# Kernel optimization log

Measured on AMD Instinct MI355X. Metric: run time of the kernel, lower is better.

Reference implementation:

```python
import jax, jax.numpy as jnp
import numpy as np

DT = 0.001  # fixed dt in SimplifiedSSM.forward
LN_EPS = 1e-5


def _layernorm(x, g, b):
    m = jnp.mean(x, axis=-1, keepdims=True)
    v = jnp.mean(jnp.square(x - m), axis=-1, keepdims=True)
    return (x - m) * jax.lax.rsqrt(v + LN_EPS) * g + b


def setup_inputs() -> dict:
    key = jax.random.key(0)
    ks = jax.random.split(key, 12)
    Bn, C, H, W = 8, 1024, 32, 32
    depth, S = 4, 128
    d = C
    inp = {
        "x": jax.random.normal(ks[0], (Bn, C, H, W), dtype=jnp.float32),
        # SSM params, stacked over depth. A scaled by 0.1 for numerical stability
        # of the length-1024 recurrence (same math, tamer eigenvalues).
        "A": 0.1 * jax.random.normal(ks[1], (depth, S, S), dtype=jnp.float32),
        "Bp": jax.random.normal(ks[2], (depth, S, d), dtype=jnp.float32),
        "Cp": jax.random.normal(ks[3], (depth, d, S), dtype=jnp.float32),
        "Dp": jax.random.normal(ks[4], (depth, d), dtype=jnp.float32),
        # Linear layers (PyTorch convention: y = x @ W.T + b)
        "Wi": jax.random.normal(ks[5], (depth, d, d), dtype=jnp.float32) / np.sqrt(d),
        "bi": jax.random.normal(ks[6], (depth, d), dtype=jnp.float32) * 0.01,
        "Wo": jax.random.normal(ks[7], (depth, d, d), dtype=jnp.float32) / np.sqrt(d),
        "bo": jax.random.normal(ks[8], (depth, d), dtype=jnp.float32) * 0.01,
        # LayerNorm affine params
        "gamma": jnp.ones((depth, d), dtype=jnp.float32),
        "beta": jnp.zeros((depth, d), dtype=jnp.float32),
    }
    return inp


def reference(x, A, Bp, Cp, Dp, Wi, bi, Wo, bo, gamma, beta):
    Bn, C, H, W = x.shape
    depth, S, _ = A.shape
    # b c h w -> b (h w) c
    seq = x.reshape(Bn, C, H * W).transpose(0, 2, 1)
    eye = jnp.eye(S, dtype=x.dtype)
    for i in range(depth):
        n = _layernorm(seq, gamma[i], beta[i])
        u = n @ Wi[i].T + bi[i]                       # (B, L, d)
        A_bar = eye + DT * A[i]                       # (S, S)
        ub = jnp.einsum('bld,sd->lbs', u, DT * Bp[i]) # (L, B, S)

        def step(h, ub_t):
            h = h @ A_bar.T + ub_t
            return h, h

        h0 = jnp.zeros((Bn, S), dtype=x.dtype)
        _, hs = jax.lax.scan(step, h0, ub)            # hs: (L, B, S)
        y = jnp.einsum('lbs,ds->bld', hs, Cp[i]) + u * Dp[i]
        seq = seq + y @ Wo[i].T + bo[i]
    return seq.transpose(0, 2, 1).reshape(Bn, C, H, W)
```

## Files before the change

kernel.cpp:

```cpp
#include <hip/hip_runtime.h>
#include <stdint.h>

#define DT_STEP 0.001f
#define LN_EPS  1e-5f
#define Bn      8
#define Lseq    1024
#define Dm      1024
#define Sn      128
#define DEPTH   4
#define Mrows   (Bn * Lseq)
#define Qc      32
#define NCHUNK  (Lseq / Qc)
#define NPOW    33

typedef short bf16x8 __attribute__((ext_vector_type(8)));
typedef float f32x4  __attribute__((ext_vector_type(4)));

__device__ __forceinline__ unsigned short f2bf(float f) {
    unsigned int u = __float_as_uint(f);
    u += 0x7fffu + ((u >> 16) & 1u);
    return (unsigned short)(u >> 16);
}

#define GLOAD_LDS16(gp, lp)                                                \
    __builtin_amdgcn_global_load_lds(                                      \
        (const __attribute__((address_space(1))) unsigned int*)(gp),       \
        (__attribute__((address_space(3))) unsigned int*)(lp), 16, 0, 0)

__global__ __launch_bounds__(256) void f2bf_kernel(const float* __restrict__ src,
                                                   unsigned short* __restrict__ dst,
                                                   int n) {
    int i = (blockIdx.x * 256 + threadIdx.x) * 4;
    if (i < n) {
        float4 v = *(const float4*)(src + i);
        ushort4 o;
        o.x = f2bf(v.x); o.y = f2bf(v.y); o.z = f2bf(v.z); o.w = f2bf(v.w);
        *(ushort4*)(dst + i) = o;
    }
}

__global__ __launch_bounds__(256) void convscale_kernel(const float* __restrict__ Wo,
                                                        const float* __restrict__ Dp,
                                                        unsigned short* __restrict__ dst) {
    int z = blockIdx.y;
    int i = (blockIdx.x * 256 + threadIdx.x) * 4;
    const float* S = Wo + (size_t)z * Dm * Dm;
    const float* dp = Dp + (size_t)z * Dm;
    float4 v = *(const float4*)(S + i);
    int c = i & (Dm - 1);
    float4 d = *(const float4*)(dp + c);
    ushort4 o;
    o.x = f2bf(v.x * d.x); o.y = f2bf(v.y * d.y);
    o.z = f2bf(v.z * d.z); o.w = f2bf(v.w * d.w);
    *(ushort4*)(dst + (size_t)z * Dm * Dm + i) = o;
}

__global__ __launch_bounds__(256) void transpose_f2bf(const float* __restrict__ src,
                                                      unsigned short* __restrict__ dst,
                                                      int R, int C) {
    __shared__ float t[32][33];
    int z = blockIdx.z;
    const float* S = src + (size_t)z * R * C;
    unsigned short* D = dst + (size_t)z * R * C;
    int r0 = blockIdx.y * 32, c0 = blockIdx.x * 32;
    int tx = threadIdx.x & 31, ty = threadIdx.x >> 5;
    for (int rr = ty; rr < 32; rr += 8)
        t[rr][tx] = S[(size_t)(r0 + rr) * C + c0 + tx];
    __syncthreads();
    for (int rr = ty; rr < 32; rr += 8)
        D[(size_t)(c0 + rr) * R + r0 + tx] = f2bf(t[tx][rr]);
}

__global__ __launch_bounds__(256) void c2dt_kernel(const float* __restrict__ Bp,
                                                   const float* __restrict__ bi,
                                                   float* __restrict__ c2dt) {
    int z = blockIdx.x, s = blockIdx.y;
    int tid = threadIdx.x;
    const float* br = Bp + ((size_t)z * Sn + s) * Dm;
    const float* bb = bi + (size_t)z * Dm;
    float4 v = *(const float4*)(br + tid * 4);
    float4 w = *(const float4*)(bb + tid * 4);
    float acc = v.x * w.x + v.y * w.y + v.z * w.z + v.w * w.w;
#pragma unroll
    for (int off = 32; off > 0; off >>= 1) acc += __shfl_down(acc, off, 64);
    __shared__ float red[4];
    if ((tid & 63) == 0) red[tid >> 6] = acc;
    __syncthreads();
    if (tid == 0) c2dt[z * Sn + s] = DT_STEP * (red[0] + red[1] + red[2] + red[3]);
}

__global__ __launch_bounds__(256) void boeff_kernel(const float* __restrict__ Wo,
                                                    const float* __restrict__ Dp,
                                                    const float* __restrict__ bi,
                                                    const float* __restrict__ bo,
                                                    float* __restrict__ boeff) {
    int z = blockIdx.x, c = blockIdx.y;
    int tid = threadIdx.x;
    const float* wr = Wo + ((size_t)z * Dm + c) * Dm;
    const float* dp = Dp + (size_t)z * Dm;
    const float* bb = bi + (size_t)z * Dm;
    float4 w = *(const float4*)(wr + tid * 4);
    float4 d = *(const float4*)(dp + tid * 4);
    float4 b = *(const float4*)(bb + tid * 4);
    float acc = w.x * d.x * b.x + w.y * d.y * b.y + w.z * d.z * b.z + w.w * d.w * b.w;
#pragma unroll
    for (int off = 32; off > 0; off >>= 1) acc += __shfl_down(acc, off, 64);
    __shared__ float red[4];
    if ((tid & 63) == 0) red[tid >> 6] = acc;
    __syncthreads();
    if (tid == 0)
        boeff[(size_t)z * Dm + c] =
            bo[(size_t)z * Dm + c] + red[0] + red[1] + red[2] + red[3];
}

__global__ __launch_bounds__(1024) void transpose_bll(const float* __restrict__ src,
                                                      float* __restrict__ dst) {
    __shared__ float tile[32][33];
    int b  = blockIdx.z;
    int i0 = blockIdx.y * 32, j0 = blockIdx.x * 32;
    int tx = threadIdx.x, ty = threadIdx.y;
    const float* S = src + (size_t)b * Dm * Lseq;
    float*       D = dst + (size_t)b * Dm * Lseq;
    tile[ty][tx] = S[(size_t)(j0 + ty) * 1024 + i0 + tx];
    __syncthreads();
    D[(size_t)(i0 + ty) * 1024 + j0 + tx] = tile[tx][ty];
}

__global__ __launch_bounds__(256) void ln_kernel(const float* __restrict__ x,
                                                 unsigned short* __restrict__ outp,
                                                 const float* __restrict__ g,
                                                 const float* __restrict__ bta) {
    int row = blockIdx.x;
    int tid = threadIdx.x;
    const float* xr = x + (size_t)row * Dm;
    float4 v = *(const float4*)(xr + tid * 4);
    float s  = v.x + v.y + v.z + v.w;
    float ss = v.x * v.x + v.y * v.y + v.z * v.z + v.w * v.w;
#pragma unroll
    for (int off = 32; off > 0; off >>= 1) {
        s  += __shfl_down(s, off, 64);
        ss += __shfl_down(ss, off, 64);
    }
    __shared__ float red[8];
    __shared__ float mv[2];
    int wave = tid >> 6, lane = tid & 63;
    if (lane == 0) { red[wave] = s; red[4 + wave] = ss; }
    __syncthreads();
    if (tid == 0) {
        float st  = red[0] + red[1] + red[2] + red[3];
        float sst = red[4] + red[5] + red[6] + red[7];
        float mean = st / (float)Dm;
        float var  = sst / (float)Dm - mean * mean;
        mv[0] = mean;
        mv[1] = rsqrtf(var + LN_EPS);
    }
    __syncthreads();
    float mean = mv[0], rstd = mv[1];
    int c = tid * 4;
    float4 gv = *(const float4*)(g + c);
    float4 bv = *(const float4*)(bta + c);
    ushort4 o;
    o.x = f2bf((v.x - mean) * rstd * gv.x + bv.x);
    o.y = f2bf((v.y - mean) * rstd * gv.y + bv.y);
    o.z = f2bf((v.z - mean) * rstd * gv.z + bv.z);
    o.w = f2bf((v.w - mean) * rstd * gv.w + bv.w);
    *(ushort4*)(outp + (size_t)row * Dm + c) = o;
}

__global__ __launch_bounds__(512) void gemm_bk64(
    const unsigned short* __restrict__ A1, int sA1,
    const unsigned short* __restrict__ A2, int sA2, int KA1,
    const unsigned short* __restrict__ B1, int sB1,
    const unsigned short* __restrict__ B2, int sB2,
    float* __restrict__ Cf, unsigned short* __restrict__ Ch,
    const float* __restrict__ bias1, const float* __restrict__ bias2,
    int ny, int N, int K, float scale, int mode,
    long batchA, long batchB, long batchC) {
    __shared__ __align__(16) unsigned short As[1024 * 8];
    __shared__ __align__(16) unsigned short Bs[1024 * 8];
    int flat = blockIdx.x;
    int rb = flat % ny, cb = flat / ny;
    int row0 = rb * 128, col0 = cb * 128;
    int z = blockIdx.y;
    int tid  = threadIdx.x;
    int wave = tid >> 6, lane = tid & 63;
    int wm = (wave & 1) * 64, wn = (wave >> 1) * 32;
    int lr = lane & 15, lq = lane >> 4;

    int rowS[2], kclS[2], slotOff[2];
#pragma unroll
    for (int q = 0; q < 2; q++) {
        int s = tid + q * 512;
        rowS[q] = s >> 3;
        kclS[q] = (s & 7) ^ ((s >> 3) & 7);
        slotOff[q] = s * 8;
    }
    int aoff[4][2], boff[2][2];
#pragma unroll
    for (int i = 0; i < 4; i++)
#pragma unroll
        for (int h = 0; h < 2; h++) {
            int ra = wm + i * 16 + lr;
            aoff[i][h] = (ra * 8 + ((lq + 4 * h) ^ (ra & 7))) * 8;
        }
#pragma unroll
    for (int j = 0; j < 2; j++)
#pragma unroll
        for (int h = 0; h < 2; h++) {
            int rn = wn + j * 16 + lr;
            boff[j][h] = (rn * 8 + ((lq + 4 * h) ^ (rn & 7))) * 8;
        }

    const unsigned short* A1b = A1 + (size_t)z * batchA;
    const unsigned short* BfixBlk = nullptr;
    int sBfix = sB1;
    if (mode == 0) {
        if (col0 < N - 128) { BfixBlk = B1 + (size_t)col0 * sB1; sBfix = sB1; }
        else                { BfixBlk = B2;                      sBfix = sB2; }
    } else if (mode == 2) {
        BfixBlk = B1 + (size_t)z * batchB + (size_t)col0 * sB1;
        sBfix = sB1;
    }

    f32x4 acc[4][2];
#pragma unroll
    for (int i = 0; i < 4; i++)
#pragma unroll
        for (int j = 0; j < 2; j++) acc[i][j] = (f32x4){0.f, 0.f, 0.f, 0.f};

    for (int k0 = 0; k0 < K; k0 += 64) {
        const unsigned short *Ab, *Bb;
        int sa, sb, ko;
        if (mode == 1) {
            if (k0 < KA1) { Ab = A1; sa = sA1; Bb = B1 + (size_t)col0 * sB1; sb = sB1; ko = k0; }
            else          { Ab = A2; sa = sA2; Bb = B2 + (size_t)col0 * sB2; sb = sB2; ko = k0 - KA1; }
        } else {
            Ab = A1b; sa = sA1; Bb = BfixBlk; sb = sBfix; ko = k0;
        }
        const unsigned short* Abr = Ab + (size_t)row0 * sa + ko;
        const unsigned short* Bbr = Bb + ko;
        __syncthreads();
#pragma unroll
        for (int q = 0; q < 2; q++) {
            GLOAD_LDS16(Abr + (size_t)rowS[q] * sa + kclS[q] * 8, &As[slotOff[q]]);
            GLOAD_LDS16(Bbr + (size_t)rowS[q] * sb + kclS[q] * 8, &Bs[slotOff[q]]);
        }
        __syncthreads();
#pragma unroll
        for (int h = 0; h < 2; h++) {
            bf16x8 af[4], bfr[2];
#pragma unroll
            for (int i = 0; i < 4; i++) af[i]  = *(const bf16x8*)&As[aoff[i][h]];
#pragma unroll
            for (int j = 0; j < 2; j++) bfr[j] = *(const bf16x8*)&Bs[boff[j][h]];
#pragma unroll
            for (int i = 0; i < 4; i++)
#pragma unroll
                for (int j = 0; j < 2; j++)
                    acc[i][j] = __builtin_amdgcn_mfma_f32_16x16x32_bf16(af[i], bfr[j],
                                                                       acc[i][j], 0, 0, 0);
        }
    }
#pragma unroll
    for (int i = 0; i < 4; i++) {
#pragma unroll
        for (int j = 0; j < 2; j++) {
#pragma unroll
            for (int r = 0; r < 4; r++) {
                int row = row0 + wm + i * 16 + lq * 4 + r;
                int col = col0 + wn + j * 16 + lr;
                float v = acc[i][j][r];
                if (mode == 0) {
                    int nu = N - 128;
                    if (col < nu) {
                        Ch[(size_t)row * nu + col] = f2bf(v + bias1[col]);
                    } else {
                        int cc = col - nu;
                        Cf[(size_t)row * 128 + cc] = v + bias2[cc];
                    }
                } else if (mode == 1) {
                    size_t idx = (size_t)row * N + col;
                    Cf[idx] = Cf[idx] + v + bias1[col];
                } else {
                    Ch[(size_t)z * batchC + (size_t)row * N + col] = f2bf(v * scale);
                }
            }
        }
    }
}

__global__ __launch_bounds__(128) void pow_init(const float* __restrict__ Amat,
                                                float* __restrict__ Pow) {
    int i = blockIdx.x;
    int s = blockIdx.y;
    int k = threadIdx.x;
    float eye = (s == k) ? 1.f : 0.f;
    size_t base = (size_t)i * NPOW * (Sn * Sn);
    Pow[base + (size_t)s * Sn + k] = eye;
    Pow[base + (size_t)(Sn * Sn) + (size_t)s * Sn + k] =
        eye + DT_STEP * Amat[(size_t)i * Sn * Sn + (size_t)s * Sn + k];
}

__global__ __launch_bounds__(256) void pow_mul(float* __restrict__ Pow, int m, int kmax) {
    int job = blockIdx.z;
    int i  = job / kmax;
    int kk = job % kmax + 1;
    const float* Pa = Pow + ((size_t)i * NPOW + m) * (Sn * Sn);
    const float* Pb = Pow + ((size_t)i * NPOW + kk) * (Sn * Sn);
    float*       Pc = Pow + ((size_t)i * NPOW + m + kk) * (Sn * Sn);
    int r0 = blockIdx.y * 64, c0 = blockIdx.x * 32;
    __shared__ float Asl[64 * 129];
    __shared__ float Bsl[128 * 32];
    int tx = threadIdx.x, ty = threadIdx.y;
    int tid = ty * 16 + tx;
    for (int idx = tid; idx < 64 * 128; idx += 256) {
        int r = idx >> 7, cc = idx & 127;
        Asl[r * 129 + cc] = Pa[(size_t)(r0 + r) * 128 + cc];
    }
    for (int idx = tid; idx < 128 * 32; idx += 256) {
        int r = idx >> 5, cc = idx & 31;
        Bsl[r * 32 + cc] = Pb[(size_t)r * 128 + c0 + cc];
    }
    __syncthreads();
    float acc[4][2] = {{0.f,0.f},{0.f,0.f},{0.f,0.f},{0.f,0.f}};
    for (int k = 0; k < 128; k++) {
        float b0 = Bsl[k * 32 + tx * 2];
        float b1 = Bsl[k * 32 + tx * 2 + 1];
#pragma unroll
        for (int r = 0; r < 4; r++) {
            float a = Asl[(ty * 4 + r) * 129 + k];
            acc[r][0] += a * b0;
            acc[r][1] += a * b1;
        }
    }
#pragma unroll
    for (int r = 0; r < 4; r++) {
        Pc[(size_t)(r0 + ty * 4 + r) * 128 + c0 + tx * 2]     = acc[r][0];
        Pc[(size_t)(r0 + ty * 4 + r) * 128 + c0 + tx * 2 + 1] = acc[r][1];
    }
}

__global__ __launch_bounds__(128) void local_scan(const float* __restrict__ ub,
                                                  float* __restrict__ hs,
                                                  const float* __restrict__ Abar) {
    int b = blockIdx.x / NCHUNK;
    int c = blockIdx.x % NCHUNK;
    int s = threadIdx.x;
    float arow[Sn];
#pragma unroll
    for (int k = 0; k < Sn; k += 4) {
        float4 v = *(const float4*)(Abar + (size_t)s * Sn + k);
        arow[k] = v.x; arow[k + 1] = v.y; arow[k + 2] = v.z; arow[k + 3] = v.w;
    }
    __shared__ __align__(16) float hsh[Sn];
    hsh[s] = 0.f;
    __syncthreads();
    size_t base = (size_t)(b * Lseq + c * Qc) * Sn + s;
    for (int t = 0; t < Qc; t++) {
        float ut = ub[base + (size_t)t * Sn];
        float a0 = 0.f, a1 = 0.f, a2 = 0.f, a3 = 0.f;
#pragma unroll
        for (int k = 0; k < Sn; k += 16) {
            float4 h0 = *(const float4*)&hsh[k];
            float4 h1 = *(const float4*)&hsh[k + 4];
            float4 h2 = *(const float4*)&hsh[k + 8];
            float4 h3 = *(const float4*)&hsh[k + 12];
            a0 += arow[k + 0] * h0.x + arow[k + 1] * h0.y + arow[k + 2] * h0.z + arow[k + 3] * h0.w;
            a1 += arow[k + 4] * h1.x + arow[k + 5] * h1.y + arow[k + 6] * h1.z + arow[k + 7] * h1.w;
            a2 += arow[k + 8] * h2.x + arow[k + 9] * h2.y + arow[k + 10] * h2.z + arow[k + 11] * h2.w;
            a3 += arow[k + 12] * h3.x + arow[k + 13] * h3.y + arow[k + 14] * h3.z + arow[k + 15] * h3.w;
        }
        float hv = ut + (a0 + a1) + (a2 + a3);
        hs[base + (size_t)t * Sn] = hv;
        __syncthreads();
        hsh[s] = hv;
        __syncthreads();
    }
}

__global__ __launch_bounds__(128) void carry_scan(const float* __restrict__ hs,
                                                  const float* __restrict__ AQ,
                                                  float* __restrict__ carry) {
    int b = blockIdx.x;
    int s = threadIdx.x;
    float le[NCHUNK];
#pragma unroll
    for (int c = 0; c < NCHUNK; c++)
        le[c] = hs[(size_t)(b * Lseq + c * Qc + Qc - 1) * Sn + s];
    float arow[Sn];
#pragma unroll
    for (int k = 0; k < Sn; k += 4) {
        float4 v = *(const float4*)(AQ + (size_t)s * Sn + k);
        arow[k] = v.x; arow[k + 1] = v.y; arow[k + 2] = v.z; arow[k + 3] = v.w;
    }
    __shared__ __align__(16) float csh[Sn];
    csh[s] = 0.f;
    __syncthreads();
    for (int c = 0; c < NCHUNK; c++) {
        carry[((size_t)b * NCHUNK + c) * Sn + s] = csh[s];
        float a0 = 0.f, a1 = 0.f, a2 = 0.f, a3 = 0.f;
#pragma unroll
        for (int k = 0; k < Sn; k += 16) {
            float4 h0 = *(const float4*)&csh[k];
            float4 h1 = *(const float4*)&csh[k + 4];
            float4 h2 = *(const float4*)&csh[k + 8];
            float4 h3 = *(const float4*)&csh[k + 12];
            a0 += arow[k + 0] * h0.x + arow[k + 1] * h0.y + arow[k + 2] * h0.z + arow[k + 3] * h0.w;
            a1 += arow[k + 4] * h1.x + arow[k + 5] * h1.y + arow[k + 6] * h1.z + arow[k + 7] * h1.w;
            a2 += arow[k + 8] * h2.x + arow[k + 9] * h2.y + arow[k + 10] * h2.z + arow[k + 11] * h2.w;
            a3 += arow[k + 12] * h3.x + arow[k + 13] * h3.y + arow[k + 14] * h3.z + arow[k + 15] * h3.w;
        }
        float cv = le[c] + (a0 + a1) + (a2 + a3);
        __syncthreads();
        csh[s] = cv;
        __syncthreads();
    }
}

__global__ __launch_bounds__(256) void fixup_scan(const float* __restrict__ hs,
                                                  unsigned short* __restrict__ hs_bf,
                                                  const float* __restrict__ PowLayer,
                                                  const float* __restrict__ carry) {
    int t  = blockIdx.x;
    int c4 = blockIdx.y;
    const float* P = PowLayer + (size_t)(t + 1) * (Sn * Sn);
    __shared__ float Pl[Sn * 65];
    __shared__ float cl[4][Bn * Sn];
    int tid = threadIdx.x;
#pragma unroll
    for (int cc = 0; cc < 4; cc++)
        for (int idx = tid; idx < Bn * Sn; idx += 256)
            cl[cc][idx] = carry[((size_t)(idx >> 7) * NCHUNK + (c4 * 4 + cc)) * Sn + (idx & 127)];
    int s = tid & 127, bh = tid >> 7;
    float acc[4][4];
#pragma unroll
    for (int cc = 0; cc < 4; cc++)
#pragma unroll
        for (int j = 0; j < 4; j++) acc[cc][j] = 0.f;
    for (int kh = 0; kh < 2; kh++) {
        __syncthreads();
        for (int idx = tid; idx < Sn * 64; idx += 256) {
            int r = idx >> 6, kk = idx & 63;
            Pl[r * 65 + kk] = P[(size_t)r * Sn + kh * 64 + kk];
        }
        __syncthreads();
        for (int kk = 0; kk < 64; kk++) {
            float pw = Pl[s * 65 + kk];
            int kg = kh * 64 + kk;
#pragma unroll
            for (int cc = 0; cc < 4; cc++)
#pragma unroll
                for (int j = 0; j < 4; j++)
                    acc[cc][j] += pw * cl[cc][(bh * 4 + j) * Sn + kg];
        }
    }
#pragma unroll
    for (int cc = 0; cc < 4; cc++) {
        int c = c4 * 4 + cc;
#pragma unroll
        for (int j = 0; j < 4; j++) {
            int bb = bh * 4 + j;
            size_t rowi = (size_t)(bb * Lseq + c * Qc + t) * Sn + s;
            hs_bf[rowi] = f2bf(hs[rowi] + acc[cc][j]);
        }
    }
}

extern "C" void kernel_launch(void* const* d_in, const int* in_sizes, int n_in,
                              void* d_out, int out_size, void* d_ws, size_t ws_size,
                              hipStream_t stream) {
    const float* x     = (const float*)d_in[0];
    const float* Am    = (const float*)d_in[1];
    const float* Bp    = (const float*)d_in[2];
    const float* Cp    = (const float*)d_in[3];
    const float* Dp    = (const float*)d_in[4];
    const float* Wi    = (const float*)d_in[5];
    const float* bi    = (const float*)d_in[6];
    const float* Wo    = (const float*)d_in[7];
    const float* bo    = (const float*)d_in[8];
    const float* gamma = (const float*)d_in[9];
    const float* beta  = (const float*)d_in[10];
    float* out = (float*)d_out;
    (void)in_sizes; (void)n_in; (void)out_size; (void)ws_size;

    char* ws = (char*)d_ws;
    float*          seq   = (float*)(ws + (size_t)0);
    unsigned short* nbuf  = (unsigned short*)(ws + (size_t)33554432);
    unsigned short* WiTh  = (unsigned short*)(ws + (size_t)33554432);
    unsigned short* Woh   = (unsigned short*)(ws + (size_t)41943040);
    unsigned short* W4h   = (unsigned short*)(ws + (size_t)50331648);
    float*          boeff = (float*)(ws + (size_t)58720256);
    float*          ub    = (float*)(ws + (size_t)67108864);
    float*          hs    = (float*)(ws + (size_t)71303168);
    unsigned short* hs_bf = (unsigned short*)(ws + (size_t)75497472);
    float*          Pow   = (float*)(ws + (size_t)77594624);
    float*          carry = (float*)(ws + (size_t)86245376);
    unsigned short* Wo2h  = (unsigned short*)(ws + (size_t)94765056);
    unsigned short* Bph   = (unsigned short*)(ws + (size_t)103153664);
    unsigned short* CpTh  = (unsigned short*)(ws + (size_t)104202240);
    unsigned short* M2h   = (unsigned short*)(ws + (size_t)105250816);
    unsigned short* W3h   = (unsigned short*)(ws + (size_t)106299392);
    float*          c2dt  = (float*)(ws + (size_t)107347968);

    const long WW = (long)Dm * Dm;
    const long SW = (long)Sn * Dm;

    hipLaunchKernelGGL(f2bf_kernel, dim3(DEPTH * WW / 1024), dim3(256), 0, stream,
                       Wo, Woh, DEPTH * (int)WW);
    hipLaunchKernelGGL(f2bf_kernel, dim3(DEPTH * SW / 1024), dim3(256), 0, stream,
                       Bp, Bph, DEPTH * (int)SW);
    hipLaunchKernelGGL(convscale_kernel, dim3(WW / 1024, DEPTH), dim3(256), 0, stream,
                       Wo, Dp, Wo2h);
    hipLaunchKernelGGL(transpose_f2bf, dim3(32, 32, DEPTH), dim3(256), 0, stream,
                       Wi, WiTh, Dm, Dm);
    hipLaunchKernelGGL(transpose_f2bf, dim3(4, 32, DEPTH), dim3(256), 0, stream,
                       Cp, CpTh, Dm, Sn);
    hipLaunchKernelGGL(c2dt_kernel, dim3(DEPTH, Sn), dim3(256), 0, stream, Bp, bi, c2dt);
    hipLaunchKernelGGL(boeff_kernel, dim3(DEPTH, Dm), dim3(256), 0, stream,
                       Wo, Dp, bi, bo, boeff);

    hipLaunchKernelGGL(gemm_bk64, dim3(8, DEPTH), dim3(512), 0, stream,
                       Bph, Dm, (const unsigned short*)nullptr, 0, 0,
                       WiTh, Dm, (const unsigned short*)nullptr, 0,
                       (float*)nullptr, M2h, (const float*)nullptr, (const float*)nullptr,
                       1, Dm, Dm, DT_STEP, 2, SW, WW, SW);
    hipLaunchKernelGGL(gemm_bk64, dim3(8, DEPTH), dim3(512), 0, stream,
                       Woh, Dm, (const unsigned short*)nullptr, 0, 0,
                       CpTh, Dm, (const unsigned short*)nullptr, 0,
                       (float*)nullptr, W3h, (const float*)nullptr, (const float*)nullptr,
                       8, Sn, Dm, 1.f, 2, WW, SW, SW);
    hipLaunchKernelGGL(gemm_bk64, dim3(8 * 8, DEPTH), dim3(512), 0, stream,
                       Wo2h, Dm, (const unsigned short*)nullptr, 0, 0,
                       WiTh, Dm, (const unsigned short*)nullptr, 0,
                       (float*)nullptr, W4h, (const float*)nullptr, (const float*)nullptr,
                       8, Dm, Dm, 1.f, 2, WW, WW, WW);

    hipLaunchKernelGGL(transpose_bll, dim3(32, 32, Bn), dim3(32, 32), 0, stream, x, seq);

    hipLaunchKernelGGL(pow_init, dim3(DEPTH, Sn), dim3(Sn), 0, stream, Am, Pow);
    for (int m = 1; m < Qc; m <<= 1) {
        hipLaunchKernelGGL(pow_mul, dim3(4, 2, DEPTH * m), dim3(16, 16), 0, stream,
                           Pow, m, m);
    }

    for (int i = 0; i < DEPTH; i++) {
        const unsigned short* M2_i = M2h + (size_t)i * SW;
        const unsigned short* W3_i = W3h + (size_t)i * SW;
        const unsigned short* W4_i = W4h + (size_t)i * WW;
        const float* PowL = Pow + (size_t)i * NPOW * (Sn * Sn);

        hipLaunchKernelGGL(ln_kernel, dim3(Mrows), dim3(256), 0, stream,
                           seq, nbuf, gamma + i * Dm, beta + i * Dm);
        hipLaunchKernelGGL(gemm_bk64, dim3(64, 1), dim3(512), 0, stream,
                           nbuf, Dm, (const unsigned short*)nullptr, 0, 0,
                           (const unsigned short*)nullptr, 0, M2_i, Dm,
                           ub, (unsigned short*)nullptr, bi + i * Dm, c2dt + i * Sn,
                           64, Sn, Dm, 1.f, 0, 0, 0, 0);
        hipLaunchKernelGGL(local_scan, dim3(Bn * NCHUNK), dim3(Sn), 0, stream,
                           ub, hs, PowL + (size_t)1 * Sn * Sn);
        hipLaunchKernelGGL(carry_scan, dim3(Bn), dim3(Sn), 0, stream,
                           hs, PowL + (size_t)Qc * Sn * Sn, carry);
        hipLaunchKernelGGL(fixup_scan, dim3(Qc, NCHUNK / 4), dim3(256), 0, stream,
                           hs, hs_bf, PowL, carry);
        hipLaunchKernelGGL(gemm_bk64, dim3(8 * 64, 1), dim3(512), 0, stream,
                           hs_bf, Sn, nbuf, Dm, Sn,
                           W3_i, Sn, W4_i, Dm,
                           seq, (unsigned short*)nullptr, boeff + i * Dm, (const float*)nullptr,
                           64, Dm, Dm + Sn, 1.f, 1, 0, 0, 0);
    }

    hipLaunchKernelGGL(transpose_bll, dim3(32, 32, Bn), dim3(32, 32), 0, stream, seq, out);
}
```

Before: 810.7 us.

## Fuse LayerNorm, ub projection GEMM and local chunk scan into one kernel

Replaces the per-layer ln_kernel, the ub GEMM and local_scan with one fused kernel. Each 128-row block computes LN statistics, normalizes into LDS while writing nbuf, runs the 128x128 MFMA projection, and performs the four 32-step chunk scans straight from LDS. This drops the ub round trip through global memory and two launches per layer. The setup conversion and bias kernels are also merged to cut launch count. The fused kernel runs only 64 blocks with large LDS use, so the GPU may be underfilled compared with the separate launches.

After: 891.7 us. 1.1x slower.

```diff
diff --git a/kernel.cpp b/kernel.cpp
--- a/kernel.cpp
+++ b/kernel.cpp
@@ -27,32 +27,33 @@
         (const __attribute__((address_space(1))) unsigned int*)(gp),       \
         (__attribute__((address_space(3))) unsigned int*)(lp), 16, 0, 0)
 
-__global__ __launch_bounds__(256) void f2bf_kernel(const float* __restrict__ src,
-                                                   unsigned short* __restrict__ dst,
-                                                   int n) {
-    int i = (blockIdx.x * 256 + threadIdx.x) * 4;
-    if (i < n) {
-        float4 v = *(const float4*)(src + i);
+__global__ __launch_bounds__(256) void prep_conv(const float* __restrict__ Wo,
+                                                 const float* __restrict__ Dp,
+                                                 const float* __restrict__ Bp,
+                                                 unsigned short* __restrict__ Woh,
+                                                 unsigned short* __restrict__ Wo2h,
+                                                 unsigned short* __restrict__ Bph) {
+    int z = blockIdx.y;
+    int bx = blockIdx.x;
+    if (bx < 1024) {
+        int i = (bx * 256 + threadIdx.x) * 4;
+        const float* S = Wo + (size_t)z * Dm * Dm;
+        float4 v = *(const float4*)(S + i);
+        int c = i & (Dm - 1);
+        float4 d = *(const float4*)(Dp + (size_t)z * Dm + c);
+        ushort4 o1, o2;
+        o1.x = f2bf(v.x); o1.y = f2bf(v.y); o1.z = f2bf(v.z); o1.w = f2bf(v.w);
+        o2.x = f2bf(v.x * d.x); o2.y = f2bf(v.y * d.y);
+        o2.z = f2bf(v.z * d.z); o2.w = f2bf(v.w * d.w);
+        *(ushort4*)(Woh  + (size_t)z * Dm * Dm + i) = o1;
+        *(ushort4*)(Wo2h + (size_t)z * Dm * Dm + i) = o2;
+    } else {
+        int i = ((bx - 1024) * 256 + threadIdx.x) * 4;
+        float4 v = *(const float4*)(Bp + (size_t)z * Sn * Dm + i);
         ushort4 o;
         o.x = f2bf(v.x); o.y = f2bf(v.y); o.z = f2bf(v.z); o.w = f2bf(v.w);
-        *(ushort4*)(dst + i) = o;
-    }
-}
-
-__global__ __launch_bounds__(256) void convscale_kernel(const float* __restrict__ Wo,
-                                                        const float* __restrict__ Dp,
-                                                        unsigned short* __restrict__ dst) {
-    int z = blockIdx.y;
-    int i = (blockIdx.x * 256 + threadIdx.x) * 4;
-    const float* S = Wo + (size_t)z * Dm * Dm;
-    const float* dp = Dp + (size_t)z * Dm;
-    float4 v = *(const float4*)(S + i);
-    int c = i & (Dm - 1);
-    float4 d = *(const float4*)(dp + c);
-    ushort4 o;
-    o.x = f2bf(v.x * d.x); o.y = f2bf(v.y * d.y);
-    o.z = f2bf(v.z * d.z); o.w = f2bf(v.w * d.w);
-    *(ushort4*)(dst + (size_t)z * Dm * Dm + i) = o;
+        *(ushort4*)(Bph + (size_t)z * Sn * Dm + i) = o;
+    }
 }
 
 __global__ __launch_bounds__(256) void transpose_f2bf(const float* __restrict__ src,
@@ -71,46 +72,42 @@
         D[(size_t)(c0 + rr) * R + r0 + tx] = f2bf(t[tx][rr]);
 }
 
-__global__ __launch_bounds__(256) void c2dt_kernel(const float* __restrict__ Bp,
-                                                   const float* __restrict__ bi,
-                                                   float* __restrict__ c2dt) {
-    int z = blockIdx.x, s = blockIdx.y;
+__global__ __launch_bounds__(256) void c2dt_boeff(const float* __restrict__ Bp,
+                                                  const float* __restrict__ bi,
+                                                  const float* __restrict__ Wo,
+                                                  const float* __restrict__ Dp,
+                                                  const float* __restrict__ bo,
+                                                  float* __restrict__ c2dt,
+                                                  float* __restrict__ boeff) {
+    int z = blockIdx.x, j = blockIdx.y;
     int tid = threadIdx.x;
-    const float* br = Bp + ((size_t)z * Sn + s) * Dm;
-    const float* bb = bi + (size_t)z * Dm;
-    float4 v = *(const float4*)(br + tid * 4);
-    float4 w = *(const float4*)(bb + tid * 4);
-    float acc = v.x * w.x + v.y * w.y + v.z * w.z + v.w * w.w;
+    float acc;
+    if (j < Sn) {
+        const float* br = Bp + ((size_t)z * Sn + j) * Dm;
+        const float* bb = bi + (size_t)z * Dm;
+        float4 v = *(const float4*)(br + tid * 4);
+        float4 w = *(const float4*)(bb + tid * 4);
+        acc = v.x * w.x + v.y * w.y + v.z * w.z + v.w * w.w;
+    } else {
+        int c = j - Sn;
+        const float* wr = Wo + ((size_t)z * Dm + c) * Dm;
+        const float* dp = Dp + (size_t)z * Dm;
+        const float* bb = bi + (size_t)z * Dm;
+        float4 w = *(const float4*)(wr + tid * 4);
+        float4 d = *(const float4*)(dp + tid * 4);
+        float4 b = *(const float4*)(bb + tid * 4);
+        acc = w.x * d.x * b.x + w.y * d.y * b.y + w.z * d.z * b.z + w.w * d.w * b.w;
+    }
 #pragma unroll
     for (int off = 32; off > 0; off >>= 1) acc += __shfl_down(acc, off, 64);
     __shared__ float red[4];
     if ((tid & 63) == 0) red[tid >> 6] = acc;
     __syncthreads();
-    if (tid == 0) c2dt[z * Sn + s] = DT_STEP * (red[0] + red[1] + red[2] + red[3]);
-}
-
-__global__ __launch_bounds__(256) void boeff_kernel(const float* __restrict__ Wo,
-                                                    const float* __restrict__ Dp,
-                                                    const float* __restrict__ bi,
-                                                    const float* __restrict__ bo,
-                                                    float* __restrict__ boeff) {
-    int z = blockIdx.x, c = blockIdx.y;
-    int tid = threadIdx.x;
-    const float* wr = Wo + ((size_t)z * Dm + c) * Dm;
-    const float* dp = Dp + (size_t)z * Dm;
-    const float* bb = bi + (size_t)z * Dm;
-    float4 w = *(const float4*)(wr + tid * 4);
-    float4 d = *(const float4*)(dp + tid * 4);
-    float4 b = *(const float4*)(bb + tid * 4);
-    float acc = w.x * d.x * b.x + w.y * d.y * b.y + w.z * d.z * b.z + w.w * d.w * b.w;
-#pragma unroll
-    for (int off = 32; off > 0; off >>= 1) acc += __shfl_down(acc, off, 64);
-    __shared__ float red[4];
-    if ((tid & 63) == 0) red[tid >> 6] = acc;
-    __syncthreads();
-    if (tid == 0)
-        boeff[(size_t)z * Dm + c] =
-            bo[(size_t)z * Dm + c] + red[0] + red[1] + red[2] + red[3];
+    if (tid == 0) {
+        float tot = red[0] + red[1] + red[2] + red[3];
+        if (j < Sn) c2dt[z * Sn + j] = DT_STEP * tot;
+        else        boeff[(size_t)z * Dm + (j - Sn)] = bo[(size_t)z * Dm + (j - Sn)] + tot;
+    }
 }
 
 __global__ __launch_bounds__(1024) void transpose_bll(const float* __restrict__ src,
@@ -126,45 +123,175 @@
     D[(size_t)(i0 + ty) * 1024 + j0 + tx] = tile[tx][ty];
 }
 
-__global__ __launch_bounds__(256) void ln_kernel(const float* __restrict__ x,
-                                                 unsigned short* __restrict__ outp,
-                                                 const float* __restrict__ g,
-                                                 const float* __restrict__ bta) {
-    int row = blockIdx.x;
-    int tid = threadIdx.x;
-    const float* xr = x + (size_t)row * Dm;
-    float4 v = *(const float4*)(xr + tid * 4);
-    float s  = v.x + v.y + v.z + v.w;
-    float ss = v.x * v.x + v.y * v.y + v.z * v.z + v.w * v.w;
-#pragma unroll
-    for (int off = 32; off > 0; off >>= 1) {
-        s  += __shfl_down(s, off, 64);
-        ss += __shfl_down(ss, off, 64);
-    }
-    __shared__ float red[8];
-    __shared__ float mv[2];
+__global__ __launch_bounds__(512) void fused_front(
+    const float* __restrict__ seq,
+    unsigned short* __restrict__ nbuf,
+    float* __restrict__ hs,
+    const unsigned short* __restrict__ M2,
+    const float* __restrict__ gam,
+    const float* __restrict__ bet,
+    const float* __restrict__ c2dtL,
+    const float* __restrict__ Abar) {
+    __shared__ __align__(16) unsigned short As[1024 * 8];
+    __shared__ __align__(16) unsigned short Bs[1024 * 8];
+    __shared__ __align__(16) float ubl[128 * 129];
+    __shared__ float mrow[128], rrow[128], cdt[128];
+    __shared__ __align__(16) float hsh[4 * 128];
+
+    int beta = blockIdx.x;
+    int row0 = beta * 128;
+    int tid  = threadIdx.x;
     int wave = tid >> 6, lane = tid & 63;
-    if (lane == 0) { red[wave] = s; red[4 + wave] = ss; }
+    int wm = (wave & 1) * 64, wn = (wave >> 1) * 32;
+    int lr = lane & 15, lq = lane >> 4;
+
+    {
+        int r = tid >> 2, q = tid & 3;
+        const float* xr = seq + (size_t)(row0 + r) * Dm;
+        float s = 0.f, ss = 0.f;
+        for (int j = 0; j < 64; j++) {
+            float4 v = *(const float4*)(xr + j * 16 + q * 4);
+            s  += v.x + v.y + v.z + v.w;
+            ss += v.x * v.x + v.y * v.y + v.z * v.z + v.w * v.w;
+        }
+        s  += __shfl_xor(s, 1, 64);  ss += __shfl_xor(ss, 1, 64);
+        s  += __shfl_xor(s, 2, 64);  ss += __shfl_xor(ss, 2, 64);
+        if (q == 0) {
+            float mean = s / (float)Dm;
+            float var  = ss / (float)Dm - mean * mean;
+            mrow[r] = mean;
+            rrow[r] = rsqrtf(var + LN_EPS);
+        }
+        if (tid < 128) cdt[tid] = c2dtL[tid];
+    }
+
+    int rowS[2], kclS[2], slotOff[2];
+#pragma unroll
+    for (int q = 0; q < 2; q++) {
+        int s = tid + q * 512;
+        rowS[q] = s >> 3;
+        kclS[q] = (s & 7) ^ ((s >> 3) & 7);
+        slotOff[q] = s * 8;
+    }
+    int aoff[4][2], boff[2][2];
+#pragma unroll
+    for (int i = 0; i < 4; i++)
+#pragma unroll
+        for (int h = 0; h < 2; h++) {
+            int ra = wm + i * 16 + lr;
+            aoff[i][h] = (ra * 8 + ((lq + 4 * h) ^ (ra & 7))) * 8;
+        }
+#pragma unroll
+    for (int j = 0; j < 2; j++)
+#pragma unroll
+        for (int h = 0; h < 2; h++) {
+            int rn = wn + j * 16 + lr;
+            boff[j][h] = (rn * 8 + ((lq + 4 * h) ^ (rn & 7))) * 8;
+        }
+
+    f32x4 acc[4][2];
+#pragma unroll
+    for (int i = 0; i < 4; i++)
+#pragma unroll
+        for (int j = 0; j < 2; j++) acc[i][j] = (f32x4){0.f, 0.f, 0.f, 0.f};
+
+    for (int k0 = 0; k0 < Dm; k0 += 64) {
+        __syncthreads();
+#pragma unroll
+        for (int q = 0; q < 2; q++)
+            GLOAD_LDS16(M2 + (size_t)rowS[q] * Dm + k0 + kclS[q] * 8, &Bs[slotOff[q]]);
+#pragma unroll
+        for (int q = 0; q < 2; q++) {
+            int gi = tid * 2 + q;
+            int rA = gi >> 3, kc = gi & 7;
+            int col = k0 + kc * 8;
+            const float* p = seq + (size_t)(row0 + rA) * Dm + col;
+            float4 v0 = *(const float4*)(p);
+            float4 v1 = *(const float4*)(p + 4);
+            float m = mrow[rA], rs = rrow[rA];
+            float4 g0 = *(const float4*)(gam + col);
+            float4 g1 = *(const float4*)(gam + col + 4);
+            float4 b0 = *(const float4*)(bet + col);
+            float4 b1 = *(const float4*)(bet + col + 4);
+            bf16x8 pk;
+            pk[0] = (short)f2bf((v0.x - m) * rs * g0.x + b0.x);
+            pk[1] = (short)f2bf((v0.y - m) * rs * g0.y + b0.y);
+            pk[2] = (short)f2bf((v0.z - m) * rs * g0.z + b0.z);
+            pk[3] = (short)f2bf((v0.w - m) * rs * g0.w + b0.w);
+            pk[4] = (short)f2bf((v1.x - m) * rs * g1.x + b1.x);
+            pk[5] = (short)f2bf((v1.y - m) * rs * g1.y + b1.y);
+            pk[6] = (short)f2bf((v1.z - m) * rs * g1.z + b1.z);
+            pk[7] = (short)f2bf((v1.w - m) * rs * g1.w + b1.w);
+            int slot = rA * 8 + (kc ^ (rA & 7));
+            *(bf16x8*)&As[slot * 8] = pk;
+            *(bf16x8*)(nbuf + (size_t)(row0 + rA) * Dm + col) = pk;
+        }
+        __syncthreads();
+#pragma unroll
+        for (int h = 0; h < 2; h++) {
+            bf16x8 af[4], bfr[2];
+#pragma unroll
+            for (int i = 0; i < 4; i++) af[i]  = *(const bf16x8*)&As[aoff[i][h]];
+#pragma unroll
+            for (int j = 0; j < 2; j++) bfr[j] = *(const bf16x8*)&Bs[boff[j][h]];
+#pragma unroll
+            for (int i = 0; i < 4; i++)
+#pragma unroll
+                for (int j = 0; j < 2; j++)
+                    acc[i][j] = __builtin_amdgcn_mfma_f32_16x16x32_bf16(af[i], bfr[j],
+                                                                       acc[i][j], 0, 0, 0);
+        }
+    }
+
+#pragma unroll
+    for (int i = 0; i < 4; i++)
+#pragma unroll
+        for (int j = 0; j < 2; j++)
+#pragma unroll
+            for (int r = 0; r < 4; r++) {
+                int rl = wm + i * 16 + lq * 4 + r;
+                int cl = wn + j * 16 + lr;
+                ubl[rl * 129 + cl] = acc[i][j][r] + cdt[cl];
+            }
+    {
+        int s = tid & 127, cc = tid >> 7;
+        hsh[cc * 128 + s] = 0.f;
+    }
     __syncthreads();
-    if (tid == 0) {
-        float st  = red[0] + red[1] + red[2] + red[3];
-        float sst = red[4] + red[5] + red[6] + red[7];
-        float mean = st / (float)Dm;
-        float var  = sst / (float)Dm - mean * mean;
-        mv[0] = mean;
-        mv[1] = rsqrtf(var + LN_EPS);
-    }
-    __syncthreads();
-    float mean = mv[0], rstd = mv[1];
-    int c = tid * 4;
-    float4 gv = *(const float4*)(g + c);
-    float4 bv = *(const float4*)(bta + c);
-    ushort4 o;
-    o.x = f2bf((v.x - mean) * rstd * gv.x + bv.x);
-    o.y = f2bf((v.y - mean) * rstd * gv.y + bv.y);
-    o.z = f2bf((v.z - mean) * rstd * gv.z + bv.z);
-    o.w = f2bf((v.w - mean) * rstd * gv.w + bv.w);
-    *(ushort4*)(outp + (size_t)row * Dm + c) = o;
+
+    {
+        int s = tid & 127, cc = tid >> 7;
+        float arow[Sn];
+#pragma unroll
+        for (int k = 0; k < Sn; k += 4) {
+            float4 v = *(const float4*)(Abar + (size_t)s * Sn + k);
+            arow[k] = v.x; arow[k + 1] = v.y; arow[k + 2] = v.z; arow[k + 3] = v.w;
+        }
+        int b = beta >> 3;
+        int c = (beta & 7) * 4 + cc;
+        size_t gbase = (size_t)(b * Lseq + c * Qc) * Sn + s;
+        float* hch = &hsh[cc * 128];
+        for (int t = 0; t < Qc; t++) {
+            float ut = ubl[(cc * 32 + t) * 129 + s];
+            float a0 = 0.f, a1 = 0.f, a2 = 0.f, a3 = 0.f;
+#pragma unroll
+            for (int k = 0; k < Sn; k += 16) {
+                float4 h0 = *(const float4*)&hch[k];
+                float4 h1 = *(const float4*)&hch[k + 4];
+                float4 h2 = *(const float4*)&hch[k + 8];
+                float4 h3 = *(const float4*)&hch[k + 12];
+                a0 += arow[k + 0] * h0.x + arow[k + 1] * h0.y + arow[k + 2] * h0.z + arow[k + 3] * h0.w;
+                a1 += arow[k + 4] * h1.x + arow[k + 5] * h1.y + arow[k + 6] * h1.z + arow[k + 7] * h1.w;
+                a2 += arow[k + 8] * h2.x + arow[k + 9] * h2.y + arow[k + 10] * h2.z + arow[k + 11] * h2.w;
+                a3 += arow[k + 12] * h3.x + arow[k + 13] * h3.y + arow[k + 14] * h3.z + arow[k + 15] * h3.w;
+            }
+            float hv = ut + (a0 + a1) + (a2 + a3);
+            hs[gbase + (size_t)t * Sn] = hv;
+            __syncthreads();
+            hch[s] = hv;
+            __syncthreads();
+        }
+    }
 }
 
 __global__ __launch_bounds__(512) void gemm_bk64(
@@ -214,10 +341,7 @@
     const unsigned short* A1b = A1 + (size_t)z * batchA;
     const unsigned short* BfixBlk = nullptr;
     int sBfix = sB1;
-    if (mode == 0) {
-        if (col0 < N - 128) { BfixBlk = B1 + (size_t)col0 * sB1; sBfix = sB1; }
-        else                { BfixBlk = B2;                      sBfix = sB2; }
-    } else if (mode == 2) {
+    if (mode == 2) {
         BfixBlk = B1 + (size_t)z * batchB + (size_t)col0 * sB1;
         sBfix = sB1;
     }
@@ -270,15 +394,7 @@
                 int row = row0 + wm + i * 16 + lq * 4 + r;
                 int col = col0 + wn + j * 16 + lr;
                 float v = acc[i][j][r];
-                if (mode == 0) {
-                    int nu = N - 128;
-                    if (col < nu) {
-                        Ch[(size_t)row * nu + col] = f2bf(v + bias1[col]);
-                    } else {
-                        int cc = col - nu;
-                        Cf[(size_t)row * 128 + cc] = v + bias2[cc];
-                    }
-                } else if (mode == 1) {
+                if (mode == 1) {
                     size_t idx = (size_t)row * N + col;
                     Cf[idx] = Cf[idx] + v + bias1[col];
                 } else {
@@ -337,44 +453,6 @@
     for (int r = 0; r < 4; r++) {
         Pc[(size_t)(r0 + ty * 4 + r) * 128 + c0 + tx * 2]     = acc[r][0];
         Pc[(size_t)(r0 + ty * 4 + r) * 128 + c0 + tx * 2 + 1] = acc[r][1];
-    }
-}
-
-__global__ __launch_bounds__(128) void local_scan(const float* __restrict__ ub,
-                                                  float* __restrict__ hs,
-                                                  const float* __restrict__ Abar) {
-    int b = blockIdx.x / NCHUNK;
-    int c = blockIdx.x % NCHUNK;
-    int s = threadIdx.x;
-    float arow[Sn];
-#pragma unroll
-    for (int k = 0; k < Sn; k += 4) {
-        float4 v = *(const float4*)(Abar + (size_t)s * Sn + k);
-        arow[k] = v.x; arow[k + 1] = v.y; arow[k + 2] = v.z; arow[k + 3] = v.w;
-    }
-    __shared__ __align__(16) float hsh[Sn];
-    hsh[s] = 0.f;
-    __syncthreads();
-    size_t base = (size_t)(b * Lseq + c * Qc) * Sn + s;
-    for (int t = 0; t < Qc; t++) {
-        float ut = ub[base + (size_t)t * Sn];
-        float a0 = 0.f, a1 = 0.f, a2 = 0.f, a3 = 0.f;
-#pragma unroll
-        for (int k = 0; k < Sn; k += 16) {
-            float4 h0 = *(const float4*)&hsh[k];
-            float4 h1 = *(const float4*)&hsh[k + 4];
-            float4 h2 = *(const float4*)&hsh[k + 8];
-            float4 h3 = *(const float4*)&hsh[k + 12];
-            a0 += arow[k + 0] * h0.x + arow[k + 1] * h0.y + arow[k + 2] * h0.z + arow[k + 3] * h0.w;
-            a1 += arow[k + 4] * h1.x + arow[k + 5] * h1.y + arow[k + 6] * h1.z + arow[k + 7] * h1.w;
-            a2 += arow[k + 8] * h2.x + arow[k + 9] * h2.y + arow[k + 10] * h2.z + arow[k + 11] * h2.w;
-            a3 += arow[k + 12] * h3.x + arow[k + 13] * h3.y + arow[k + 14] * h3.z + arow[k + 15] * h3.w;
-        }
-        float hv = ut + (a0 + a1) + (a2 + a3);
-        hs[base + (size_t)t * Sn] = hv;
-        __syncthreads();
-        hsh[s] = hv;
-        __syncthreads();
     }
 }
 
@@ -490,7 +568,6 @@
     unsigned short* Woh   = (unsigned short*)(ws + (size_t)41943040);
     unsigned short* W4h   = (unsigned short*)(ws + (size_t)50331648);
     float*          boeff = (float*)(ws + (size_t)58720256);
-    float*          ub    = (float*)(ws + (size_t)67108864);
     float*          hs    = (float*)(ws + (size_t)71303168);
     unsigned short* hs_bf = (unsigned short*)(ws + (size_t)75497472);
     float*          Pow   = (float*)(ws + (size_t)77594624);
@@ -505,19 +582,14 @@
     const long WW = (long)Dm * Dm;
     const long SW = (long)Sn * Dm;
 
-    hipLaunchKernelGGL(f2bf_kernel, dim3(DEPTH * WW / 1024), dim3(256), 0, stream,
-                       Wo, Woh, DEPTH * (int)WW);
-    hipLaunchKernelGGL(f2bf_kernel, dim3(DEPTH * SW / 1024), dim3(256), 0, stream,
-                       Bp, Bph, DEPTH * (int)SW);
-    hipLaunchKernelGGL(convscale_kernel, dim3(WW / 1024, DEPTH), dim3(256), 0, stream,
-                       Wo, Dp, Wo2h);
+    hipLaunchKernelGGL(prep_conv, dim3(1024 + 128, DEPTH), dim3(256), 0, stream,
+                       Wo, Dp, Bp, Woh, Wo2h, Bph);
     hipLaunchKernelGGL(transpose_f2bf, dim3(32, 32, DEPTH), dim3(256), 0, stream,
                        Wi, WiTh, Dm, Dm);
     hipLaunchKernelGGL(transpose_f2bf, dim3(4, 32, DEPTH), dim3(256), 0, stream,
                        Cp, CpTh, Dm, Sn);
-    hipLaunchKernelGGL(c2dt_kernel, dim3(DEPTH, Sn), dim3(256), 0, stream, Bp, bi, c2dt);
-    hipLaunchKernelGGL(boeff_kernel, dim3(DEPTH, Dm), dim3(256), 0, stream,
-                       Wo, Dp, bi, bo, boeff);
+    hipLaunchKernelGGL(c2dt_boeff, dim3(DEPTH, Sn + Dm), dim3(256), 0, stream,
+                       Bp, bi, Wo, Dp, bo, c2dt, boeff);
 
     hipLaunchKernelGGL(gemm_bk64, dim3(8, DEPTH), dim3(512), 0, stream,
                        Bph, Dm, (const unsigned short*)nullptr, 0, 0,
@@ -549,15 +621,9 @@
         const unsigned short* W4_i = W4h + (size_t)i * WW;
         const float* PowL = Pow + (size_t)i * NPOW * (Sn * Sn);
 
-        hipLaunchKernelGGL(ln_kernel, dim3(Mrows), dim3(256), 0, stream,
-                           seq, nbuf, gamma + i * Dm, beta + i * Dm);
-        hipLaunchKernelGGL(gemm_bk64, dim3(64, 1), dim3(512), 0, stream,
-                           nbuf, Dm, (const unsigned short*)nullptr, 0, 0,
-                           (const unsigned short*)nullptr, 0, M2_i, Dm,
-                           ub, (unsigned short*)nullptr, bi + i * Dm, c2dt + i * Sn,
-                           64, Sn, Dm, 1.f, 0, 0, 0, 0);
-        hipLaunchKernelGGL(local_scan, dim3(Bn * NCHUNK), dim3(Sn), 0, stream,
-                           ub, hs, PowL + (size_t)1 * Sn * Sn);
+        hipLaunchKernelGGL(fused_front, dim3(64), dim3(512), 0, stream,
+                           seq, nbuf, hs, M2_i, gamma + i * Dm, beta + i * Dm,
+                           c2dt + i * Sn, PowL + (size_t)Sn * Sn);
         hipLaunchKernelGGL(carry_scan, dim3(Bn), dim3(Sn), 0, stream,
                            hs, PowL + (size_t)Qc * Sn * Sn, carry);
         hipLaunchKernelGGL(fixup_scan, dim3(Qc, NCHUNK / 4), dim3(256), 0, stream,
```

## Add dedicated skinny GEMM for ub projection and fuse setup kernels

Applied to the files above, without the earlier changes.

Replaces the generic 128x128-tile GEMM used for the Mrows x 128 ub projection, which launched only 64 blocks, with a specialised kernel that uses 32-row tiles and 256 blocks so more of the GPU is busy. It also merges the weight conversion kernels into one launch and the c2dt/boeff reductions into one launch, and prefetches the next ub value in local_scan. The new kernel does less reuse per tile and streams the full B matrix per block, which adds L2 traffic.

Result: faster. 764.4 us (-5.7%).

```diff
diff --git a/kernel.cpp b/kernel.cpp
--- a/kernel.cpp
+++ b/kernel.cpp
@@ -27,32 +27,33 @@
         (const __attribute__((address_space(1))) unsigned int*)(gp),       \
         (__attribute__((address_space(3))) unsigned int*)(lp), 16, 0, 0)
 
-__global__ __launch_bounds__(256) void f2bf_kernel(const float* __restrict__ src,
-                                                   unsigned short* __restrict__ dst,
-                                                   int n) {
-    int i = (blockIdx.x * 256 + threadIdx.x) * 4;
-    if (i < n) {
-        float4 v = *(const float4*)(src + i);
+__global__ __launch_bounds__(256) void prep_conv(const float* __restrict__ Wo,
+                                                 const float* __restrict__ Dp,
+                                                 const float* __restrict__ Bp,
+                                                 unsigned short* __restrict__ Woh,
+                                                 unsigned short* __restrict__ Wo2h,
+                                                 unsigned short* __restrict__ Bph) {
+    int z = blockIdx.y;
+    int bx = blockIdx.x;
+    if (bx < 1024) {
+        int i = (bx * 256 + threadIdx.x) * 4;
+        const float* S = Wo + (size_t)z * Dm * Dm;
+        float4 v = *(const float4*)(S + i);
+        int c = i & (Dm - 1);
+        float4 d = *(const float4*)(Dp + (size_t)z * Dm + c);
+        ushort4 o1, o2;
+        o1.x = f2bf(v.x); o1.y = f2bf(v.y); o1.z = f2bf(v.z); o1.w = f2bf(v.w);
+        o2.x = f2bf(v.x * d.x); o2.y = f2bf(v.y * d.y);
+        o2.z = f2bf(v.z * d.z); o2.w = f2bf(v.w * d.w);
+        *(ushort4*)(Woh  + (size_t)z * Dm * Dm + i) = o1;
+        *(ushort4*)(Wo2h + (size_t)z * Dm * Dm + i) = o2;
+    } else {
+        int i = ((bx - 1024) * 256 + threadIdx.x) * 4;
+        float4 v = *(const float4*)(Bp + (size_t)z * Sn * Dm + i);
         ushort4 o;
         o.x = f2bf(v.x); o.y = f2bf(v.y); o.z = f2bf(v.z); o.w = f2bf(v.w);
-        *(ushort4*)(dst + i) = o;
-    }
-}
-
-__global__ __launch_bounds__(256) void convscale_kernel(const float* __restrict__ Wo,
-                                                        const float* __restrict__ Dp,
-                                                        unsigned short* __restrict__ dst) {
-    int z = blockIdx.y;
-    int i = (blockIdx.x * 256 + threadIdx.x) * 4;
-    const float* S = Wo + (size_t)z * Dm * Dm;
-    const float* dp = Dp + (size_t)z * Dm;
-    float4 v = *(const float4*)(S + i);
-    int c = i & (Dm - 1);
-    float4 d = *(const float4*)(dp + c);
-    ushort4 o;
-    o.x = f2bf(v.x * d.x); o.y = f2bf(v.y * d.y);
-    o.z = f2bf(v.z * d.z); o.w = f2bf(v.w * d.w);
-    *(ushort4*)(dst + (size_t)z * Dm * Dm + i) = o;
+        *(ushort4*)(Bph + (size_t)z * Sn * Dm + i) = o;
+    }
 }
 
 __global__ __launch_bounds__(256) void transpose_f2bf(const float* __restrict__ src,
@@ -71,46 +72,42 @@
         D[(size_t)(c0 + rr) * R + r0 + tx] = f2bf(t[tx][rr]);
 }
 
-__global__ __launch_bounds__(256) void c2dt_kernel(const float* __restrict__ Bp,
-                                                   const float* __restrict__ bi,
-                                                   float* __restrict__ c2dt) {
-    int z = blockIdx.x, s = blockIdx.y;
+__global__ __launch_bounds__(256) void c2dt_boeff(const float* __restrict__ Bp,
+                                                  const float* __restrict__ bi,
+                                                  const float* __restrict__ Wo,
+                                                  const float* __restrict__ Dp,
+                                                  const float* __restrict__ bo,
+                                                  float* __restrict__ c2dt,
+                                                  float* __restrict__ boeff) {
+    int z = blockIdx.x, j = blockIdx.y;
     int tid = threadIdx.x;
-    const float* br = Bp + ((size_t)z * Sn + s) * Dm;
-    const float* bb = bi + (size_t)z * Dm;
-    float4 v = *(const float4*)(br + tid * 4);
-    float4 w = *(const float4*)(bb + tid * 4);
-    float acc = v.x * w.x + v.y * w.y + v.z * w.z + v.w * w.w;
+    float acc;
+    if (j < Sn) {
+        const float* br = Bp + ((size_t)z * Sn + j) * Dm;
+        const float* bb = bi + (size_t)z * Dm;
+        float4 v = *(const float4*)(br + tid * 4);
+        float4 w = *(const float4*)(bb + tid * 4);
+        acc = v.x * w.x + v.y * w.y + v.z * w.z + v.w * w.w;
+    } else {
+        int c = j - Sn;
+        const float* wr = Wo + ((size_t)z * Dm + c) * Dm;
+        const float* dp = Dp + (size_t)z * Dm;
+        const float* bb = bi + (size_t)z * Dm;
+        float4 w = *(const float4*)(wr + tid * 4);
+        float4 d = *(const float4*)(dp + tid * 4);
+        float4 b = *(const float4*)(bb + tid * 4);
+        acc = w.x * d.x * b.x + w.y * d.y * b.y + w.z * d.z * b.z + w.w * d.w * b.w;
+    }
 #pragma unroll
     for (int off = 32; off > 0; off >>= 1) acc += __shfl_down(acc, off, 64);
     __shared__ float red[4];
     if ((tid & 63) == 0) red[tid >> 6] = acc;
     __syncthreads();
-    if (tid == 0) c2dt[z * Sn + s] = DT_STEP * (red[0] + red[1] + red[2] + red[3]);
-}
-
-__global__ __launch_bounds__(256) void boeff_kernel(const float* __restrict__ Wo,
-                                                    const float* __restrict__ Dp,
-                                                    const float* __restrict__ bi,
-                                                    const float* __restrict__ bo,
-                                                    float* __restrict__ boeff) {
-    int z = blockIdx.x, c = blockIdx.y;
-    int tid = threadIdx.x;
-    const float* wr = Wo + ((size_t)z * Dm + c) * Dm;
-    const float* dp = Dp + (size_t)z * Dm;
-    const float* bb = bi + (size_t)z * Dm;
-    float4 w = *(const float4*)(wr + tid * 4);
-    float4 d = *(const float4*)(dp + tid * 4);
-    float4 b = *(const float4*)(bb + tid * 4);
-    float acc = w.x * d.x * b.x + w.y * d.y * b.y + w.z * d.z * b.z + w.w * d.w * b.w;
-#pragma unroll
-    for (int off = 32; off > 0; off >>= 1) acc += __shfl_down(acc, off, 64);
-    __shared__ float red[4];
-    if ((tid & 63) == 0) red[tid >> 6] = acc;
-    __syncthreads();
-    if (tid == 0)
-        boeff[(size_t)z * Dm + c] =
-            bo[(size_t)z * Dm + c] + red[0] + red[1] + red[2] + red[3];
+    if (tid == 0) {
+        float tot = red[0] + red[1] + red[2] + red[3];
+        if (j < Sn) c2dt[z * Sn + j] = DT_STEP * tot;
+        else        boeff[(size_t)z * Dm + (j - Sn)] = bo[(size_t)z * Dm + (j - Sn)] + tot;
+    }
 }
 
 __global__ __launch_bounds__(1024) void transpose_bll(const float* __restrict__ src,
@@ -165,6 +162,79 @@
     o.z = f2bf((v.z - mean) * rstd * gv.z + bv.z);
     o.w = f2bf((v.w - mean) * rstd * gv.w + bv.w);
     *(ushort4*)(outp + (size_t)row * Dm + c) = o;
+}
+
+__global__ __launch_bounds__(512) void gemm_ub(
+    const unsigned short* __restrict__ A,
+    const unsigned short* __restrict__ B,
+    float* __restrict__ ub,
+    const float* __restrict__ c2dtL) {
+    __shared__ __align__(16) unsigned short As[256 * 8];
+    __shared__ __align__(16) unsigned short Bs[1024 * 8];
+    int row0 = blockIdx.x * 32;
+    int tid  = threadIdx.x;
+    int wave = tid >> 6, lane = tid & 63;
+    int wn = wave * 16;
+    int lr = lane & 15, lq = lane >> 4;
+
+    int rowA = tid >> 3;
+    int kclA = (tid & 7) ^ ((tid >> 3) & 7);
+    int rowS[2], kclS[2], slotOff[2];
+#pragma unroll
+    for (int q = 0; q < 2; q++) {
+        int s = tid + q * 512;
+        rowS[q] = s >> 3;
+        kclS[q] = (s & 7) ^ ((s >> 3) & 7);
+        slotOff[q] = s * 8;
+    }
+    int aoff[2][2], boff[2];
+#pragma unroll
+    for (int i = 0; i < 2; i++)
+#pragma unroll
+        for (int h = 0; h < 2; h++) {
+            int ra = i * 16 + lr;
+            aoff[i][h] = (ra * 8 + ((lq + 4 * h) ^ (ra & 7))) * 8;
+        }
+#pragma unroll
+    for (int h = 0; h < 2; h++) {
+        int rn = wn + lr;
+        boff[h] = (rn * 8 + ((lq + 4 * h) ^ (rn & 7))) * 8;
+    }
+
+    f32x4 acc[2];
+#pragma unroll
+    for (int i = 0; i < 2; i++) acc[i] = (f32x4){0.f, 0.f, 0.f, 0.f};
+
+    for (int k0 = 0; k0 < Dm; k0 += 64) {
+        const unsigned short* Abr = A + (size_t)row0 * Dm + k0;
+        const unsigned short* Bbr = B + k0;
+        __syncthreads();
+        if (tid < 256)
+            GLOAD_LDS16(Abr + (size_t)rowA * Dm + kclA * 8, &As[tid * 8]);
+#pragma unroll
+        for (int q = 0; q < 2; q++)
+            GLOAD_LDS16(Bbr + (size_t)rowS[q] * Dm + kclS[q] * 8, &Bs[slotOff[q]]);
+        __syncthreads();
+#pragma unroll
+        for (int h = 0; h < 2; h++) {
+            bf16x8 af[2], bfr;
+#pragma unroll
+            for (int i = 0; i < 2; i++) af[i] = *(const bf16x8*)&As[aoff[i][h]];
+            bfr = *(const bf16x8*)&Bs[boff[h]];
+#pragma unroll
+            for (int i = 0; i < 2; i++)
+                acc[i] = __builtin_amdgcn_mfma_f32_16x16x32_bf16(af[i], bfr,
+                                                                 acc[i], 0, 0, 0);
+        }
+    }
+#pragma unroll
+    for (int i = 0; i < 2; i++)
+#pragma unroll
+        for (int r = 0; r < 4; r++) {
+            int row = row0 + i * 16 + lq * 4 + r;
+            int col = wn + lr;
+            ub[(size_t)row * Sn + col] = acc[i][r] + c2dtL[col];
+        }
 }
 
 __global__ __launch_bounds__(512) void gemm_bk64(
@@ -214,10 +284,7 @@
     const unsigned short* A1b = A1 + (size_t)z * batchA;
     const unsigned short* BfixBlk = nullptr;
     int sBfix = sB1;
-    if (mode == 0) {
-        if (col0 < N - 128) { BfixBlk = B1 + (size_t)col0 * sB1; sBfix = sB1; }
-        else                { BfixBlk = B2;                      sBfix = sB2; }
-    } else if (mode == 2) {
+    if (mode == 2) {
         BfixBlk = B1 + (size_t)z * batchB + (size_t)col0 * sB1;
         sBfix = sB1;
     }
@@ -270,15 +337,7 @@
                 int row = row0 + wm + i * 16 + lq * 4 + r;
                 int col = col0 + wn + j * 16 + lr;
                 float v = acc[i][j][r];
-                if (mode == 0) {
-                    int nu = N - 128;
-                    if (col < nu) {
-                        Ch[(size_t)row * nu + col] = f2bf(v + bias1[col]);
-                    } else {
-                        int cc = col - nu;
-                        Cf[(size_t)row * 128 + cc] = v + bias2[cc];
-                    }
-                } else if (mode == 1) {
+                if (mode == 1) {
                     size_t idx = (size_t)row * N + col;
                     Cf[idx] = Cf[idx] + v + bias1[col];
                 } else {
@@ -356,8 +415,9 @@
     hsh[s] = 0.f;
     __syncthreads();
     size_t base = (size_t)(b * Lseq + c * Qc) * Sn + s;
+    float ut = ub[base];
     for (int t = 0; t < Qc; t++) {
-        float ut = ub[base + (size_t)t * Sn];
+        float utn = (t + 1 < Qc) ? ub[base + (size_t)(t + 1) * Sn] : 0.f;
         float a0 = 0.f, a1 = 0.f, a2 = 0.f, a3 = 0.f;
 #pragma unroll
         for (int k = 0; k < Sn; k += 16) {
@@ -375,6 +435,7 @@
         __syncthreads();
         hsh[s] = hv;
         __syncthreads();
+        ut = utn;
     }
 }
 
@@ -505,19 +566,14 @@
     const long WW = (long)Dm * Dm;
     const long SW = (long)Sn * Dm;
 
-    hipLaunchKernelGGL(f2bf_kernel, dim3(DEPTH * WW / 1024), dim3(256), 0, stream,
-                       Wo, Woh, DEPTH * (int)WW);
-    hipLaunchKernelGGL(f2bf_kernel, dim3(DEPTH * SW / 1024), dim3(256), 0, stream,
-                       Bp, Bph, DEPTH * (int)SW);
-    hipLaunchKernelGGL(convscale_kernel, dim3(WW / 1024, DEPTH), dim3(256), 0, stream,
-                       Wo, Dp, Wo2h);
+    hipLaunchKernelGGL(prep_conv, dim3(1024 + 128, DEPTH), dim3(256), 0, stream,
+                       Wo, Dp, Bp, Woh, Wo2h, Bph);
     hipLaunchKernelGGL(transpose_f2bf, dim3(32, 32, DEPTH), dim3(256), 0, stream,
                        Wi, WiTh, Dm, Dm);
     hipLaunchKernelGGL(transpose_f2bf, dim3(4, 32, DEPTH), dim3(256), 0, stream,
                        Cp, CpTh, Dm, Sn);
-    hipLaunchKernelGGL(c2dt_kernel, dim3(DEPTH, Sn), dim3(256), 0, stream, Bp, bi, c2dt);
-    hipLaunchKernelGGL(boeff_kernel, dim3(DEPTH, Dm), dim3(256), 0, stream,
-                       Wo, Dp, bi, bo, boeff);
+    hipLaunchKernelGGL(c2dt_boeff, dim3(DEPTH, Sn + Dm), dim3(256), 0, stream,
+                       Bp, bi, Wo, Dp, bo, c2dt, boeff);
 
     hipLaunchKernelGGL(gemm_bk64, dim3(8, DEPTH), dim3(512), 0, stream,
                        Bph, Dm, (const unsigned short*)nullptr, 0, 0,
@@ -551,11 +607,8 @@
 
         hipLaunchKernelGGL(ln_kernel, dim3(Mrows), dim3(256), 0, stream,
                            seq, nbuf, gamma + i * Dm, beta + i * Dm);
-        hipLaunchKernelGGL(gemm_bk64, dim3(64, 1), dim3(512), 0, stream,
-                           nbuf, Dm, (const unsigned short*)nullptr, 0, 0,
-                           (const unsigned short*)nullptr, 0, M2_i, Dm,
-                           ub, (unsigned short*)nullptr, bi + i * Dm, c2dt + i * Sn,
-                           64, Sn, Dm, 1.f, 0, 0, 0, 0);
+        hipLaunchKernelGGL(gemm_ub, dim3(Mrows / 32), dim3(512), 0, stream,
+                           nbuf, M2_i, ub, c2dt + i * Sn);
         hipLaunchKernelGGL(local_scan, dim3(Bn * NCHUNK), dim3(Sn), 0, stream,
                            ub, hs, PowL + (size_t)1 * Sn * Sn);
         hipLaunchKernelGGL(carry_scan, dim3(Bn), dim3(Sn), 0, stream,
```
